# Performance work log

Measured on AMD Instinct MI355X. Metric: run time of the kernel, lower is better.

## Reference

```python
import jax, jax.numpy as jnp
import numpy as np
from functools import partial

V, BS, L, H, C = 50257, 1024, 6, 12, 768
HD = C // H

def _ln(x, w, b):
    mu = jnp.mean(x, axis=-1, keepdims=True)
    var = jnp.var(x, axis=-1, keepdims=True)
    return (x - mu) * jax.lax.rsqrt(var + 1e-5) * w + b

def setup_inputs() -> dict:
    key = jax.random.key(0)
    ks = jax.random.split(key, 12)
    s = 0.02
    inp = {
        "idx": jax.random.randint(ks[0], (4, 1024), 0, V, dtype=jnp.int32),
        "wte": jax.random.normal(ks[1], (V, C), jnp.float32) * s,
        "wpe": jax.random.normal(ks[2], (BS, C), jnp.float32) * s,
        # per-block stacked params; linear weights stored [in, out]
        "ln1_w": jnp.ones((L, C)), "ln1_b": jnp.zeros((L, C)),
        "attn_w": jax.random.normal(ks[3], (L, C, 3 * C), jnp.float32) * s,
        "attn_b": jnp.zeros((L, 3 * C)),
        "proj_w": jax.random.normal(ks[4], (L, C, C), jnp.float32) * s,
        "proj_b": jnp.zeros((L, C)),
        "ln2_w": jnp.ones((L, C)), "ln2_b": jnp.zeros((L, C)),
        "fc_w": jax.random.normal(ks[5], (L, C, 4 * C), jnp.float32) * s,
        "fc_b": jnp.zeros((L, 4 * C)),
        "fc2_w": jax.random.normal(ks[6], (L, 4 * C, C), jnp.float32) * s,
        "fc2_b": jnp.zeros((L, C)),
        "lnf_w": jnp.ones((C,)), "lnf_b": jnp.zeros((C,)),
    }
    return inp

def _forward(idx, wte, wpe, ln1_w, ln1_b, attn_w, attn_b, proj_w, proj_b,
             ln2_w, ln2_b, fc_w, fc_b, fc2_w, fc2_b, lnf_w, lnf_b):
    B, T = idx.shape
    x = wte[idx] + wpe[:T]  # [B,T,C]
    causal = jnp.tril(jnp.ones((T, T), bool))  # [T,T]
    scale = 1.0 / np.sqrt(HD)
    neg_inf = jnp.finfo(x.dtype).min

    def block(x, p):
        l1w, l1b, aw, ab, pw, pb, l2w, l2b, fw, fb, f2w, f2b = p
        h = _ln(x, l1w, l1b)
        qkv = h @ aw + ab  # [B,T,3C]
        q, k, v = jnp.split(qkv, 3, axis=-1)
        q = q.reshape(B, T, H, HD)
        k = k.reshape(B, T, H, HD)
        v = v.reshape(B, T, H, HD)
        att = jnp.einsum('bqhd,bkhd->bhqk', q, k) * scale
        att = jnp.where(causal, att, neg_inf)
        att = jax.nn.softmax(att, axis=-1)
        y = jnp.einsum('bhqk,bkhd->bqhd', att, v).reshape(B, T, C)
        x = x + y @ pw + pb
        h = _ln(x, l2w, l2b)
        h = jax.nn.gelu(h @ fw + fb, approximate=False)  # torch nn.GELU default = exact
        x = x + h @ f2w + f2b
        return x, None

    params = (ln1_w, ln1_b, attn_w, attn_b, proj_w, proj_b,
              ln2_w, ln2_b, fc_w, fc_b, fc2_w, fc2_b)
    x, _ = jax.lax.scan(block, x, params)
    x = _ln(x, lnf_w, lnf_b)
    logits = x @ wte.T  # tied lm_head, no bias
    return logits

def reference(idx, wte, wpe, ln1_w, ln1_b, attn_w, attn_b, proj_w, proj_b,
              ln2_w, ln2_b, fc_w, fc_b, fc2_w, fc2_b, lnf_w, lnf_b):
    return _forward(idx, wte, wpe, ln1_w, ln1_b, attn_w, attn_b, proj_w, proj_b,
                    ln2_w, ln2_b, fc_w, fc_b, fc2_w, fc2_b, lnf_w, lnf_b)
```

## Files before the change

### kernel.cpp

```cpp
#include <hip/hip_runtime.h>

#define BT     4096
#define CDIM   768
#define NLAYER 6
#define NHEAD  12
#define VREAL  50257
#define VPAD   50304

typedef __bf16 bf16x8 __attribute__((ext_vector_type(8)));
typedef float  f32x4  __attribute__((ext_vector_type(4)));

__device__ __forceinline__ unsigned short f2bf(float f) {
    unsigned int u = __builtin_bit_cast(unsigned int, f);
    u += 0x7fffu + ((u >> 16) & 1u);
    return (unsigned short)(u >> 16);
}

__global__ __launch_bounds__(256) void transpose_conv(
    const float* __restrict__ in, unsigned short* __restrict__ out, int K, int N)
{
    in  += (size_t)blockIdx.z * K * N;
    out += (size_t)blockIdx.z * K * N;
    __shared__ float t[32][33];
    int j0 = blockIdx.x * 32;
    int i0 = blockIdx.y * 32;
    int c = threadIdx.x;
    int r = threadIdx.y;
    #pragma unroll
    for (int rr = r; rr < 32; rr += 8)
        t[rr][c] = in[(size_t)(i0 + rr) * N + j0 + c];
    __syncthreads();
    #pragma unroll
    for (int rr = r; rr < 32; rr += 8)
        out[(size_t)(j0 + rr) * K + i0 + c] = f2bf(t[c][rr]);
}

__global__ __launch_bounds__(256) void wteconv(
    const float* __restrict__ wte, unsigned short* __restrict__ out)
{
    size_t e = ((size_t)blockIdx.x * 256 + threadIdx.x) * 4;
    int row = (int)(e / CDIM);
    int col = (int)(e % CDIM);
    ushort4 o;
    if (row < VREAL) {
        float4 v = *(const float4*)(wte + (size_t)row * CDIM + col);
        o.x = f2bf(v.x); o.y = f2bf(v.y); o.z = f2bf(v.z); o.w = f2bf(v.w);
    } else {
        o.x = 0; o.y = 0; o.z = 0; o.w = 0;
    }
    *(ushort4*)(out + e) = o;
}

__global__ __launch_bounds__(256) void embed_kernel(
    const int* __restrict__ idx, const float* __restrict__ wte,
    const float* __restrict__ wpe, float* __restrict__ x)
{
    int row = blockIdx.x;
    int t = row & 1023;
    int id = idx[row];
    const float* s = wte + (size_t)id * CDIM;
    const float* p = wpe + (size_t)t * CDIM;
    float* o = x + (size_t)row * CDIM;
    for (int c = threadIdx.x; c < CDIM; c += 256) o[c] = s[c] + p[c];
}

__global__ __launch_bounds__(256) void ln_kernel(
    const float* __restrict__ x, const float* __restrict__ w,
    const float* __restrict__ b, unsigned short* __restrict__ out)
{
    int row = blockIdx.x * 4 + (threadIdx.x >> 6);
    int lane = threadIdx.x & 63;
    const float* xp = x + (size_t)row * CDIM;
    float v[12];
    float s = 0.f, sq = 0.f;
    #pragma unroll
    for (int j = 0; j < 12; ++j) {
        float t = xp[j * 64 + lane];
        v[j] = t; s += t; sq += t * t;
    }
    #pragma unroll
    for (int o = 32; o > 0; o >>= 1) {
        s  += __shfl_xor(s, o, 64);
        sq += __shfl_xor(sq, o, 64);
    }
    float mu  = s * (1.f / CDIM);
    float var = sq * (1.f / CDIM) - mu * mu;
    float rs  = rsqrtf(var + 1e-5f);
    unsigned short* op = out + (size_t)row * CDIM;
    #pragma unroll
    for (int j = 0; j < 12; ++j) {
        int c = j * 64 + lane;
        op[c] = f2bf((v[j] - mu) * rs * w[c] + b[c]);
    }
}

template<int MODE>
__global__ __launch_bounds__(256) void gemm_kernel(
    const unsigned short* __restrict__ A, const unsigned short* __restrict__ Bt,
    const float* __restrict__ bias, const float* __restrict__ resid,
    float* __restrict__ outF, unsigned short* __restrict__ outB,
    unsigned short* __restrict__ qout, unsigned short* __restrict__ kout,
    unsigned short* __restrict__ vtout,
    int K, int Nout)
{
    __shared__ alignas(16) unsigned short As[4096];
    __shared__ alignas(16) unsigned short Bs[4096];
    const int tid  = threadIdx.x;
    const int wv   = tid >> 6;
    const int lane = tid & 63;
    const int m0 = blockIdx.x * 128;
    const int n0 = blockIdx.y * 128;
    const int wr = wv >> 1, wc = wv & 1;
    const int srow = lane >> 2;
    const int skk  = (lane & 3) * 8;
    const int fr = lane & 15;
    const int fk = (lane >> 4) * 8;

    f32x4 acc[4][4];
    #pragma unroll
    for (int i = 0; i < 4; ++i)
        #pragma unroll
        for (int j = 0; j < 4; ++j) acc[i][j] = f32x4{0.f, 0.f, 0.f, 0.f};

    for (int k0 = 0; k0 < K; k0 += 32) {
        #pragma unroll
        for (int j = 0; j < 2; ++j) {
            int row = j * 64 + wv * 16 + srow;
            const unsigned short* ga = A  + (size_t)(m0 + row) * K + k0 + skk;
            const unsigned short* gb = Bt + (size_t)(n0 + row) * K + k0 + skk;
            unsigned short* la = &As[j * 2048 + wv * 512];
            unsigned short* lb = &Bs[j * 2048 + wv * 512];
            __builtin_amdgcn_global_load_lds(
                (const __attribute__((address_space(1))) unsigned int*)ga,
                (__attribute__((address_space(3))) unsigned int*)la, 16, 0, 0);
            __builtin_amdgcn_global_load_lds(
                (const __attribute__((address_space(1))) unsigned int*)gb,
                (__attribute__((address_space(3))) unsigned int*)lb, 16, 0, 0);
        }
        __syncthreads();
        bf16x8 a[4], bb[4];
        #pragma unroll
        for (int m = 0; m < 4; ++m)
            a[m] = *(const bf16x8*)&As[(wr * 64 + m * 16 + fr) * 32 + fk];
        #pragma unroll
        for (int n = 0; n < 4; ++n)
            bb[n] = *(const bf16x8*)&Bs[(wc * 64 + n * 16 + fr) * 32 + fk];
        #pragma unroll
        for (int m = 0; m < 4; ++m)
            #pragma unroll
            for (int n = 0; n < 4; ++n)
                acc[m][n] = __builtin_amdgcn_mfma_f32_16x16x32_bf16(
                    a[m], bb[n], acc[m][n], 0, 0, 0);
        __syncthreads();
    }

    const int colb = n0 + wc * 64 + fr;
    const int rowb = m0 + wr * 64 + (lane >> 4) * 4;
    #pragma unroll
    for (int m = 0; m < 4; ++m) {
        #pragma unroll
        for (int n = 0; n < 4; ++n) {
            int col = colb + n * 16;
            int which = col / 768;
            int hh = (col - which * 768) >> 6;
            int dd = col & 63;
            #pragma unroll
            for (int r = 0; r < 4; ++r) {
                int row = rowb + m * 16 + r;
                float v = acc[m][n][r];
                if (MODE == 1) {
                    outF[(size_t)row * Nout + col] =
                        resid[(size_t)row * Nout + col] + v + bias[col];
                } else if (MODE == 2) {
                    float u = v + bias[col];
                    float g = 0.5f * u * (1.f + erff(u * 0.70710678118654752f));
                    outB[(size_t)row * Nout + col] = f2bf(g);
                } else if (MODE == 3) {
                    if (col < Nout) outF[(size_t)row * Nout + col] = v;
                } else if (MODE == 4) {
                    int bb2 = row >> 10, tt = row & 1023;
                    unsigned short val = f2bf(v + bias[col]);
                    if (which == 0)
                        qout[(((size_t)bb2 * NHEAD + hh) * 1024 + tt) * 64 + dd] = val;
                    else if (which == 1)
                        kout[(((size_t)bb2 * NHEAD + hh) * 1024 + tt) * 64 + dd] = val;
                    else
                        vtout[(((size_t)bb2 * NHEAD + hh) * 64 + dd) * 1024 + tt] = val;
                }
            }
        }
    }
}

__global__ __launch_bounds__(256) void attn_mfma_kernel(
    const unsigned short* __restrict__ qb, const unsigned short* __restrict__ kb,
    const unsigned short* __restrict__ vtb, unsigned short* __restrict__ y)
{
    __shared__ alignas(16) unsigned short Ps[4][16][72];
    const int qt = 15 - blockIdx.x;
    const int h = blockIdx.y, b = blockIdx.z;
    const int w = threadIdx.x >> 6, lane = threadIdx.x & 63;
    const int fr = lane & 15;
    const int fg = lane >> 4;
    const size_t bh = (size_t)(b * NHEAD + h);
    const unsigned short* Qb = qb  + bh * 1024 * 64;
    const unsigned short* Kb = kb  + bh * 1024 * 64;
    const unsigned short* Vt = vtb + bh * 64 * 1024;
    const int q0 = qt * 64 + w * 16;

    bf16x8 aq[2];
    aq[0] = *(const bf16x8*)(Qb + (size_t)(q0 + fr) * 64 + fg * 8);
    aq[1] = *(const bf16x8*)(Qb + (size_t)(q0 + fr) * 64 + 32 + fg * 8);

    f32x4 o[4];
    #pragma unroll
    for (int c = 0; c < 4; ++c) o[c] = f32x4{0.f, 0.f, 0.f, 0.f};
    float m[4], l[4];
    #pragma unroll
    for (int r = 0; r < 4; ++r) { m[r] = -1e30f; l[r] = 0.f; }

    for (int kt = 0; kt <= qt; ++kt) {
        const unsigned short* Kt = Kb + (size_t)kt * 64 * 64;
        f32x4 s[4];
        #pragma unroll
        for (int c = 0; c < 4; ++c) {
            bf16x8 bk0 = *(const bf16x8*)(Kt + (size_t)(c * 16 + fr) * 64 + fg * 8);
            bf16x8 bk1 = *(const bf16x8*)(Kt + (size_t)(c * 16 + fr) * 64 + 32 + fg * 8);
            s[c] = f32x4{0.f, 0.f, 0.f, 0.f};
            s[c] = __builtin_amdgcn_mfma_f32_16x16x32_bf16(aq[0], bk0, s[c], 0, 0, 0);
            s[c] = __builtin_amdgcn_mfma_f32_16x16x32_bf16(aq[1], bk1, s[c], 0, 0, 0);
        }
        float sc[4][4];
        #pragma unroll
        for (int c = 0; c < 4; ++c)
            #pragma unroll
            for (int r = 0; r < 4; ++r) {
                float v = s[c][r] * 0.125f;
                if (kt == qt && (kt * 64 + c * 16 + fr) > (q0 + fg * 4 + r))
                    v = -1e30f;
                sc[c][r] = v;
            }
        #pragma unroll
        for (int r = 0; r < 4; ++r) {
            float tm = fmaxf(fmaxf(sc[0][r], sc[1][r]), fmaxf(sc[2][r], sc[3][r]));
            tm = fmaxf(tm, __shfl_xor(tm, 1, 64));
            tm = fmaxf(tm, __shfl_xor(tm, 2, 64));
            tm = fmaxf(tm, __shfl_xor(tm, 4, 64));
            tm = fmaxf(tm, __shfl_xor(tm, 8, 64));
            float mn = fmaxf(m[r], tm);
            float corr = __expf(m[r] - mn);
            m[r] = mn;
            float ps = 0.f;
            #pragma unroll
            for (int c = 0; c < 4; ++c) {
                float p = __expf(sc[c][r] - mn);
                sc[c][r] = p;
                ps += p;
            }
            ps += __shfl_xor(ps, 1, 64);
            ps += __shfl_xor(ps, 2, 64);
            ps += __shfl_xor(ps, 4, 64);
            ps += __shfl_xor(ps, 8, 64);
            l[r] = l[r] * corr + ps;
            #pragma unroll
            for (int c = 0; c < 4; ++c) o[c][r] *= corr;
            #pragma unroll
            for (int c = 0; c < 4; ++c)
                Ps[w][fg * 4 + r][c * 16 + fr] = f2bf(sc[c][r]);
        }
        asm volatile("s_waitcnt lgkmcnt(0)" ::: "memory");
        bf16x8 ap0 = *(const bf16x8*)&Ps[w][fr][fg * 8];
        bf16x8 ap1 = *(const bf16x8*)&Ps[w][fr][32 + fg * 8];
        #pragma unroll
        for (int c = 0; c < 4; ++c) {
            const unsigned short* vb = Vt + (size_t)(c * 16 + fr) * 1024 + kt * 64;
            bf16x8 bv0 = *(const bf16x8*)(vb + fg * 8);
            bf16x8 bv1 = *(const bf16x8*)(vb + 32 + fg * 8);
            o[c] = __builtin_amdgcn_mfma_f32_16x16x32_bf16(ap0, bv0, o[c], 0, 0, 0);
            o[c] = __builtin_amdgcn_mfma_f32_16x16x32_bf16(ap1, bv1, o[c], 0, 0, 0);
        }
        asm volatile("s_waitcnt lgkmcnt(0)" ::: "memory");
    }

    float inv[4];
    #pragma unroll
    for (int r = 0; r < 4; ++r) inv[r] = 1.f / l[r];
    #pragma unroll
    for (int c = 0; c < 4; ++c)
        #pragma unroll
        for (int r = 0; r < 4; ++r) {
            int q = q0 + fg * 4 + r;
            y[((size_t)(b * 1024 + q)) * CDIM + h * 64 + c * 16 + fr] =
                f2bf(o[c][r] * inv[r]);
        }
}

extern "C" void kernel_launch(void* const* d_in, const int* in_sizes, int n_in,
                              void* d_out, int out_size, void* d_ws, size_t ws_size,
                              hipStream_t stream) {
    (void)in_sizes; (void)n_in; (void)out_size; (void)ws_size;
    const int*   idx   = (const int*)  d_in[0];
    const float* wte   = (const float*)d_in[1];
    const float* wpe   = (const float*)d_in[2];
    const float* ln1w  = (const float*)d_in[3];
    const float* ln1b  = (const float*)d_in[4];
    const float* attnw = (const float*)d_in[5];
    const float* attnb = (const float*)d_in[6];
    const float* projw = (const float*)d_in[7];
    const float* projb = (const float*)d_in[8];
    const float* ln2w  = (const float*)d_in[9];
    const float* ln2b  = (const float*)d_in[10];
    const float* fcw   = (const float*)d_in[11];
    const float* fcb   = (const float*)d_in[12];
    const float* fc2w  = (const float*)d_in[13];
    const float* fc2b  = (const float*)d_in[14];
    const float* lnfw  = (const float*)d_in[15];
    const float* lnfb  = (const float*)d_in[16];
    float* out = (float*)d_out;

    char* ws = (char*)d_ws;
    size_t off = 0;
    auto alloc = [&](size_t bytes) {
        void* p = ws + off;
        off += (bytes + 255) & ~(size_t)255;
        return p;
    };
    float*          x      = (float*)         alloc((size_t)BT * CDIM * 4);
    unsigned short* hbuf   = (unsigned short*)alloc((size_t)BT * CDIM * 2);
    unsigned short* qbuf   = (unsigned short*)alloc((size_t)BT * CDIM * 2);
    unsigned short* kbuf   = (unsigned short*)alloc((size_t)BT * CDIM * 2);
    unsigned short* vtbuf  = (unsigned short*)alloc((size_t)BT * CDIM * 2);
    unsigned short* ybuf   = (unsigned short*)alloc((size_t)BT * CDIM * 2);
    unsigned short* fcact  = (unsigned short*)alloc((size_t)BT * 4 * CDIM * 2);
    unsigned short* wqkvT  = (unsigned short*)alloc((size_t)NLAYER * 3 * CDIM * CDIM * 2);
    unsigned short* wprojT = (unsigned short*)alloc((size_t)NLAYER * CDIM * CDIM * 2);
    unsigned short* wfcT   = (unsigned short*)alloc((size_t)NLAYER * 4 * CDIM * CDIM * 2);
    unsigned short* wfc2T  = (unsigned short*)alloc((size_t)NLAYER * 4 * CDIM * CDIM * 2);
    unsigned short* wteB   = (unsigned short*)alloc((size_t)VPAD * CDIM * 2);

    transpose_conv<<<dim3(3*CDIM/32,   CDIM/32, NLAYER), dim3(32,8), 0, stream>>>(attnw, wqkvT, CDIM, 3*CDIM);
    transpose_conv<<<dim3(  CDIM/32,   CDIM/32, NLAYER), dim3(32,8), 0, stream>>>(projw, wprojT, CDIM, CDIM);
    transpose_conv<<<dim3(4*CDIM/32,   CDIM/32, NLAYER), dim3(32,8), 0, stream>>>(fcw,  wfcT,  CDIM, 4*CDIM);
    transpose_conv<<<dim3(  CDIM/32, 4*CDIM/32, NLAYER), dim3(32,8), 0, stream>>>(fc2w, wfc2T, 4*CDIM, CDIM);
    wteconv<<<(VPAD * CDIM / 4) / 256, 256, 0, stream>>>(wte, wteB);
    embed_kernel<<<BT, 256, 0, stream>>>(idx, wte, wpe, x);

    for (int l = 0; l < NLAYER; ++l) {
        ln_kernel<<<BT/4, 256, 0, stream>>>(x, ln1w + l*CDIM, ln1b + l*CDIM, hbuf);
        gemm_kernel<4><<<dim3(BT/128, 3*CDIM/128), 256, 0, stream>>>(
            hbuf, wqkvT + (size_t)l*3*CDIM*CDIM, attnb + (size_t)l*3*CDIM,
            nullptr, nullptr, nullptr, qbuf, kbuf, vtbuf, CDIM, 3*CDIM);
        attn_mfma_kernel<<<dim3(16, NHEAD, 4), 256, 0, stream>>>(qbuf, kbuf, vtbuf, ybuf);
        gemm_kernel<1><<<dim3(BT/128, CDIM/128), 256, 0, stream>>>(
            ybuf, wprojT + (size_t)l*CDIM*CDIM, projb + (size_t)l*CDIM,
            x, x, nullptr, nullptr, nullptr, nullptr, CDIM, CDIM);
        ln_kernel<<<BT/4, 256, 0, stream>>>(x, ln2w + l*CDIM, ln2b + l*CDIM, hbuf);
        gemm_kernel<2><<<dim3(BT/128, 4*CDIM/128), 256, 0, stream>>>(
            hbuf, wfcT + (size_t)l*4*CDIM*CDIM, fcb + (size_t)l*4*CDIM,
            nullptr, nullptr, fcact, nullptr, nullptr, nullptr, CDIM, 4*CDIM);
        gemm_kernel<1><<<dim3(BT/128, CDIM/128), 256, 0, stream>>>(
            fcact, wfc2T + (size_t)l*4*CDIM*CDIM, fc2b + (size_t)l*CDIM,
            x, x, nullptr, nullptr, nullptr, nullptr, 4*CDIM, CDIM);
    }
    ln_kernel<<<BT/4, 256, 0, stream>>>(x, lnfw, lnfb, hbuf);
    gemm_kernel<3><<<dim3(BT/128, VPAD/128), 256, 0, stream>>>(
        hbuf, wteB, nullptr, nullptr, out, nullptr, nullptr, nullptr, nullptr, CDIM, VREAL);
}
```

Baseline: 2.404 ms.

## Add double-buffered 256x256 LM-head GEMM, pipeline all GEMMs, swizzle block order

Adds a new 256x256-tile GEMM kernel with 512 threads for the vocabulary projection and pads the vocabulary to a multiple of 256. All GEMMs now double-buffer their LDS tiles so the next K-tile's global-to-LDS load is issued before the current tile's MFMAs. A block-index swizzle remaps workgroup order to group tiles across XCDs for better L2 locality. Larger tiles raise arithmetic intensity for the dominant LM-head GEMM, at the cost of more LDS per block and possibly lower occupancy.

```diff
diff --git a/kernel.cpp b/kernel.cpp
--- a/kernel.cpp
+++ b/kernel.cpp
@@ -5,7 +5,7 @@
 #define NLAYER 6
 #define NHEAD  12
 #define VREAL  50257
-#define VPAD   50304
+#define VPAD   50432
 
 typedef __bf16 bf16x8 __attribute__((ext_vector_type(8)));
 typedef float  f32x4  __attribute__((ext_vector_type(4)));
@@ -14,6 +14,18 @@
     unsigned int u = __builtin_bit_cast(unsigned int, f);
     u += 0x7fffu + ((u >> 16) & 1u);
     return (unsigned short)(u >> 16);
+}
+
+__device__ __forceinline__ void swz_block(int &bx, int &by) {
+    int gx = gridDim.x;
+    int nwg = gx * gridDim.y;
+    if ((nwg & 7) == 0) {
+        int lin = by * gx + bx;
+        int q = nwg >> 3;
+        lin = (lin & 7) * q + (lin >> 3);
+        bx = lin % gx;
+        by = lin / gx;
+    }
 }
 
 __global__ __launch_bounds__(256) void transpose_conv(
@@ -103,48 +115,58 @@
     unsigned short* __restrict__ vtout,
     int K, int Nout)
 {
-    __shared__ alignas(16) unsigned short As[4096];
-    __shared__ alignas(16) unsigned short Bs[4096];
+    __shared__ alignas(16) unsigned short As[2][4096];
+    __shared__ alignas(16) unsigned short Bs[2][4096];
     const int tid  = threadIdx.x;
     const int wv   = tid >> 6;
     const int lane = tid & 63;
-    const int m0 = blockIdx.x * 128;
-    const int n0 = blockIdx.y * 128;
+    int bx = blockIdx.x, by = blockIdx.y;
+    swz_block(bx, by);
+    const int m0 = bx * 128;
+    const int n0 = by * 128;
     const int wr = wv >> 1, wc = wv & 1;
     const int srow = lane >> 2;
     const int skk  = (lane & 3) * 8;
     const int fr = lane & 15;
     const int fk = (lane >> 4) * 8;
 
-    f32x4 acc[4][4];
-    #pragma unroll
-    for (int i = 0; i < 4; ++i)
-        #pragma unroll
-        for (int j = 0; j < 4; ++j) acc[i][j] = f32x4{0.f, 0.f, 0.f, 0.f};
-
-    for (int k0 = 0; k0 < K; k0 += 32) {
+    auto stage = [&](int k0, int bb) {
         #pragma unroll
         for (int j = 0; j < 2; ++j) {
             int row = j * 64 + wv * 16 + srow;
             const unsigned short* ga = A  + (size_t)(m0 + row) * K + k0 + skk;
             const unsigned short* gb = Bt + (size_t)(n0 + row) * K + k0 + skk;
-            unsigned short* la = &As[j * 2048 + wv * 512];
-            unsigned short* lb = &Bs[j * 2048 + wv * 512];
             __builtin_amdgcn_global_load_lds(
                 (const __attribute__((address_space(1))) unsigned int*)ga,
-                (__attribute__((address_space(3))) unsigned int*)la, 16, 0, 0);
+                (__attribute__((address_space(3))) unsigned int*)&As[bb][j * 2048 + wv * 512],
+                16, 0, 0);
             __builtin_amdgcn_global_load_lds(
                 (const __attribute__((address_space(1))) unsigned int*)gb,
-                (__attribute__((address_space(3))) unsigned int*)lb, 16, 0, 0);
-        }
-        __syncthreads();
+                (__attribute__((address_space(3))) unsigned int*)&Bs[bb][j * 2048 + wv * 512],
+                16, 0, 0);
+        }
+    };
+
+    f32x4 acc[4][4];
+    #pragma unroll
+    for (int i = 0; i < 4; ++i)
+        #pragma unroll
+        for (int j = 0; j < 4; ++j) acc[i][j] = f32x4{0.f, 0.f, 0.f, 0.f};
+
+    stage(0, 0);
+    __syncthreads();
+
+    const int nt = K >> 5;
+    for (int t = 0; t < nt; ++t) {
+        const int cb = t & 1;
+        if (t + 1 < nt) stage((t + 1) << 5, cb ^ 1);
         bf16x8 a[4], bb[4];
         #pragma unroll
         for (int m = 0; m < 4; ++m)
-            a[m] = *(const bf16x8*)&As[(wr * 64 + m * 16 + fr) * 32 + fk];
+            a[m] = *(const bf16x8*)&As[cb][(wr * 64 + m * 16 + fr) * 32 + fk];
         #pragma unroll
         for (int n = 0; n < 4; ++n)
-            bb[n] = *(const bf16x8*)&Bs[(wc * 64 + n * 16 + fr) * 32 + fk];
+            bb[n] = *(const bf16x8*)&Bs[cb][(wc * 64 + n * 16 + fr) * 32 + fk];
         #pragma unroll
         for (int m = 0; m < 4; ++m)
             #pragma unroll
@@ -175,8 +197,6 @@
                     float u = v + bias[col];
                     float g = 0.5f * u * (1.f + erff(u * 0.70710678118654752f));
                     outB[(size_t)row * Nout + col] = f2bf(g);
-                } else if (MODE == 3) {
-                    if (col < Nout) outF[(size_t)row * Nout + col] = v;
                 } else if (MODE == 4) {
                     int bb2 = row >> 10, tt = row & 1023;
                     unsigned short val = f2bf(v + bias[col]);
@@ -186,6 +206,93 @@
                         kout[(((size_t)bb2 * NHEAD + hh) * 1024 + tt) * 64 + dd] = val;
                     else
                         vtout[(((size_t)bb2 * NHEAD + hh) * 64 + dd) * 1024 + tt] = val;
+                }
+            }
+        }
+    }
+}
+
+__global__ __launch_bounds__(512, 2) void gemm256_kernel(
+    const unsigned short* __restrict__ A, const unsigned short* __restrict__ Bt,
+    float* __restrict__ outF, int K, int Nout)
+{
+    __shared__ alignas(16) unsigned short ldsA[2][16384];
+    __shared__ alignas(16) unsigned short ldsB[2][16384];
+    const int tid  = threadIdx.x;
+    const int wid  = tid >> 6;
+    const int lane = tid & 63;
+    int bx = blockIdx.x, by = blockIdx.y;
+    swz_block(bx, by);
+    const int m0 = bx * 256;
+    const int n0 = by * 256;
+    const int wm = wid >> 2;
+    const int wn = wid & 3;
+    const int srow = wid * 8 + (lane >> 3);
+    const int scol = (lane & 7) * 8;
+    const int fr = lane & 15;
+    const int fg = lane >> 4;
+
+    auto stage = [&](int kt, int bb) {
+        const int k0 = kt * 64;
+        #pragma unroll
+        for (int j = 0; j < 4; ++j) {
+            const unsigned short* ga = A  + (size_t)(m0 + j * 64 + srow) * K + k0 + scol;
+            const unsigned short* gb = Bt + (size_t)(n0 + j * 64 + srow) * K + k0 + scol;
+            __builtin_amdgcn_global_load_lds(
+                (const __attribute__((address_space(1))) unsigned int*)ga,
+                (__attribute__((address_space(3))) unsigned int*)&ldsA[bb][j * 4096 + wid * 512],
+                16, 0, 0);
+            __builtin_amdgcn_global_load_lds(
+                (const __attribute__((address_space(1))) unsigned int*)gb,
+                (__attribute__((address_space(3))) unsigned int*)&ldsB[bb][j * 4096 + wid * 512],
+                16, 0, 0);
+        }
+    };
+
+    f32x4 acc[8][4];
+    #pragma unroll
+    for (int i = 0; i < 8; ++i)
+        #pragma unroll
+        for (int j = 0; j < 4; ++j) acc[i][j] = f32x4{0.f, 0.f, 0.f, 0.f};
+
+    stage(0, 0);
+    __syncthreads();
+
+    const int nt = K >> 6;
+    for (int t = 0; t < nt; ++t) {
+        const int cb = t & 1;
+        if (t + 1 < nt) stage(t + 1, cb ^ 1);
+        #pragma unroll
+        for (int ks = 0; ks < 2; ++ks) {
+            bf16x8 a[8], b[4];
+            #pragma unroll
+            for (int m = 0; m < 8; ++m)
+                a[m] = *(const bf16x8*)&ldsA[cb][(wm * 128 + m * 16 + fr) * 64 + ks * 32 + fg * 8];
+            #pragma unroll
+            for (int n = 0; n < 4; ++n)
+                b[n] = *(const bf16x8*)&ldsB[cb][(wn * 64 + n * 16 + fr) * 64 + ks * 32 + fg * 8];
+            #pragma unroll
+            for (int m = 0; m < 8; ++m)
+                #pragma unroll
+                for (int n = 0; n < 4; ++n)
+                    acc[m][n] = __builtin_amdgcn_mfma_f32_16x16x32_bf16(
+                        a[m], b[n], acc[m][n], 0, 0, 0);
+        }
+        __syncthreads();
+    }
+
+    const int colb = n0 + wn * 64 + fr;
+    const int rowb = m0 + wm * 128 + fg * 4;
+    #pragma unroll
+    for (int m = 0; m < 8; ++m) {
+        #pragma unroll
+        for (int n = 0; n < 4; ++n) {
+            int col = colb + n * 16;
+            if (col < Nout) {
+                #pragma unroll
+                for (int r = 0; r < 4; ++r) {
+                    int row = rowb + m * 16 + r;
+                    outF[(size_t)row * Nout + col] = acc[m][n][r];
                 }
             }
         }
@@ -363,6 +470,6 @@
             x, x, nullptr, nullptr, nullptr, nullptr, 4*CDIM, CDIM);
     }
     ln_kernel<<<BT/4, 256, 0, stream>>>(x, lnfw, lnfb, hbuf);
-    gemm_kernel<3><<<dim3(BT/128, VPAD/128), 256, 0, stream>>>(
-        hbuf, wteB, nullptr, nullptr, out, nullptr, nullptr, nullptr, nullptr, CDIM, VREAL);
-}
+    gemm256_kernel<<<dim3(BT/256, VPAD/256), 512, 0, stream>>>(
+        hbuf, wteB, out, CDIM, VREAL);
+}
```

Result: no change. 2.451 ms (+2.0%).

## Add dedicated double-buffered LM-head GEMM kernel with swizzled LDS and block remap

Applied to the files above, without the earlier changes.

Replaces the generic gemm for the tied LM head with a specialized 512-thread kernel using 128x256 tiles. The A tile is double-buffered in LDS with XOR swizzling, and B fragments are loaded directly into registers and prefetched one step ahead. It also uses explicit waitcnt/barrier pipelining, setprio around MFMA bursts, and a workgroup remap across XCDs to improve L2 reuse. Vocabulary padding grows to a multiple of 256, which adds a little wasted compute and relies on the wteB buffer being allocated to the new VPAD size.

```diff
diff --git a/kernel.cpp b/kernel.cpp
--- a/kernel.cpp
+++ b/kernel.cpp
@@ -5,7 +5,7 @@
 #define NLAYER 6
 #define NHEAD  12
 #define VREAL  50257
-#define VPAD   50304
+#define VPAD   50432
 
 typedef __bf16 bf16x8 __attribute__((ext_vector_type(8)));
 typedef float  f32x4  __attribute__((ext_vector_type(4)));
@@ -14,6 +14,24 @@
     unsigned int u = __builtin_bit_cast(unsigned int, f);
     u += 0x7fffu + ((u >> 16) & 1u);
     return (unsigned short)(u >> 16);
+}
+
+__device__ __forceinline__ void gload16(const unsigned short* g, unsigned short* l) {
+    __builtin_amdgcn_global_load_lds(
+        (const __attribute__((address_space(1))) unsigned int*)g,
+        (__attribute__((address_space(3))) unsigned int*)l, 16, 0, 0);
+}
+
+__device__ __forceinline__ void swz_block(int &bx, int &by) {
+    int gx = gridDim.x;
+    int nwg = gx * gridDim.y;
+    if ((nwg & 7) == 0) {
+        int lin = by * gx + bx;
+        int q = nwg >> 3;
+        lin = (lin & 7) * q + (lin >> 3);
+        bx = lin % gx;
+        by = lin / gx;
+    }
 }
 
 __global__ __launch_bounds__(256) void transpose_conv(
@@ -126,16 +144,8 @@
         #pragma unroll
         for (int j = 0; j < 2; ++j) {
             int row = j * 64 + wv * 16 + srow;
-            const unsigned short* ga = A  + (size_t)(m0 + row) * K + k0 + skk;
-            const unsigned short* gb = Bt + (size_t)(n0 + row) * K + k0 + skk;
-            unsigned short* la = &As[j * 2048 + wv * 512];
-            unsigned short* lb = &Bs[j * 2048 + wv * 512];
-            __builtin_amdgcn_global_load_lds(
-                (const __attribute__((address_space(1))) unsigned int*)ga,
-                (__attribute__((address_space(3))) unsigned int*)la, 16, 0, 0);
-            __builtin_amdgcn_global_load_lds(
-                (const __attribute__((address_space(1))) unsigned int*)gb,
-                (__attribute__((address_space(3))) unsigned int*)lb, 16, 0, 0);
+            gload16(A  + (size_t)(m0 + row) * K + k0 + skk, &As[j * 2048 + wv * 512]);
+            gload16(Bt + (size_t)(n0 + row) * K + k0 + skk, &Bs[j * 2048 + wv * 512]);
         }
         __syncthreads();
         bf16x8 a[4], bb[4];
@@ -175,8 +185,6 @@
                     float u = v + bias[col];
                     float g = 0.5f * u * (1.f + erff(u * 0.70710678118654752f));
                     outB[(size_t)row * Nout + col] = f2bf(g);
-                } else if (MODE == 3) {
-                    if (col < Nout) outF[(size_t)row * Nout + col] = v;
                 } else if (MODE == 4) {
                     int bb2 = row >> 10, tt = row & 1023;
                     unsigned short val = f2bf(v + bias[col]);
@@ -186,6 +194,119 @@
                         kout[(((size_t)bb2 * NHEAD + hh) * 1024 + tt) * 64 + dd] = val;
                     else
                         vtout[(((size_t)bb2 * NHEAD + hh) * 64 + dd) * 1024 + tt] = val;
+                }
+            }
+        }
+    }
+}
+
+__global__ __launch_bounds__(512, 4) void lmhead_kernel(
+    const unsigned short* __restrict__ A, const unsigned short* __restrict__ Bt,
+    float* __restrict__ outF)
+{
+    __shared__ alignas(16) unsigned short ldsA[2][8192];
+    const int tid  = threadIdx.x;
+    const int wid  = tid >> 6;
+    const int lane = tid & 63;
+    const int fr = lane & 15, fg = lane >> 4;
+    int bx = blockIdx.x, by = blockIdx.y;
+    swz_block(bx, by);
+    const int m0 = bx * 128;
+    const int n0 = by * 256;
+
+    const int sr  = tid >> 3;
+    const int sks = ((tid & 7) * 8) ^ ((sr & 7) << 3);
+    const int wbase = wid * 512;
+
+    const unsigned short* Bw = Bt + (size_t)(n0 + wid * 32 + fr) * 768 + fg * 8;
+
+    const int arow = fr * 64;
+    const int swz0 = (fg * 8) ^ ((fr & 7) << 3);
+    const int swz1 = (32 + fg * 8) ^ ((fr & 7) << 3);
+
+    f32x4 acc[8][2];
+    #pragma unroll
+    for (int m = 0; m < 8; ++m)
+        #pragma unroll
+        for (int n = 0; n < 2; ++n) acc[m][n] = f32x4{0.f, 0.f, 0.f, 0.f};
+
+    bf16x8 brE[2][2], brO[2][2];
+
+#define LM_STAGE_A(t, buf)                                                    \
+    {                                                                         \
+        const int k0_ = (t) * 64;                                             \
+        gload16(A + (size_t)(m0 +      sr) * 768 + k0_ + sks,                 \
+                &ldsA[buf][wbase]);                                           \
+        gload16(A + (size_t)(m0 + 64 + sr) * 768 + k0_ + sks,                 \
+                &ldsA[buf][4096 + wbase]);                                    \
+    }
+#define LM_LOAD_B(t, br)                                                      \
+    {                                                                         \
+        const int k0_ = (t) * 64;                                             \
+        br[0][0] = *(const bf16x8*)(Bw + k0_);                                \
+        br[0][1] = *(const bf16x8*)(Bw + k0_ + 32);                           \
+        br[1][0] = *(const bf16x8*)(Bw + (size_t)16 * 768 + k0_);             \
+        br[1][1] = *(const bf16x8*)(Bw + (size_t)16 * 768 + k0_ + 32);        \
+    }
+#define LM_COMPUTE(buf, br)                                                   \
+    {                                                                         \
+        _Pragma("unroll")                                                     \
+        for (int m = 0; m < 8; ++m) {                                         \
+            bf16x8 a0 = *(const bf16x8*)&ldsA[buf][m * 1024 + arow + swz0];   \
+            bf16x8 a1 = *(const bf16x8*)&ldsA[buf][m * 1024 + arow + swz1];   \
+            acc[m][0] = __builtin_amdgcn_mfma_f32_16x16x32_bf16(a0, br[0][0], acc[m][0], 0, 0, 0); \
+            acc[m][1] = __builtin_amdgcn_mfma_f32_16x16x32_bf16(a0, br[1][0], acc[m][1], 0, 0, 0); \
+            acc[m][0] = __builtin_amdgcn_mfma_f32_16x16x32_bf16(a1, br[0][1], acc[m][0], 0, 0, 0); \
+            acc[m][1] = __builtin_amdgcn_mfma_f32_16x16x32_bf16(a1, br[1][1], acc[m][1], 0, 0, 0); \
+        }                                                                     \
+    }
+
+    LM_STAGE_A(0, 0);
+    LM_LOAD_B(0, brE);
+
+    #pragma unroll 1
+    for (int tt = 0; tt < 12; tt += 2) {
+        LM_STAGE_A(tt + 1, 1);
+        LM_LOAD_B(tt + 1, brO);
+        asm volatile("s_waitcnt vmcnt(6)" ::: "memory");
+        __builtin_amdgcn_s_barrier();
+        __builtin_amdgcn_s_setprio(1);
+        LM_COMPUTE(0, brE);
+        __builtin_amdgcn_s_setprio(0);
+        asm volatile("s_waitcnt lgkmcnt(0)" ::: "memory");
+        __builtin_amdgcn_sched_barrier(0);
+        __builtin_amdgcn_s_barrier();
+        if (tt + 2 < 12) {
+            LM_STAGE_A(tt + 2, 0);
+            LM_LOAD_B(tt + 2, brE);
+            asm volatile("s_waitcnt vmcnt(6)" ::: "memory");
+        } else {
+            asm volatile("s_waitcnt vmcnt(0)" ::: "memory");
+        }
+        __builtin_amdgcn_s_barrier();
+        __builtin_amdgcn_s_setprio(1);
+        LM_COMPUTE(1, brO);
+        __builtin_amdgcn_s_setprio(0);
+        asm volatile("s_waitcnt lgkmcnt(0)" ::: "memory");
+        __builtin_amdgcn_sched_barrier(0);
+        __builtin_amdgcn_s_barrier();
+    }
+#undef LM_STAGE_A
+#undef LM_LOAD_B
+#undef LM_COMPUTE
+
+    const int colb = n0 + wid * 32 + fr;
+    const int rowb = m0 + fg * 4;
+    #pragma unroll
+    for (int m = 0; m < 8; ++m) {
+        #pragma unroll
+        for (int n = 0; n < 2; ++n) {
+            int col = colb + n * 16;
+            if (col < VREAL) {
+                #pragma unroll
+                for (int r = 0; r < 4; ++r) {
+                    int row = rowb + m * 16 + r;
+                    outF[(size_t)row * VREAL + col] = acc[m][n][r];
                 }
             }
         }
@@ -363,6 +484,5 @@
             x, x, nullptr, nullptr, nullptr, nullptr, 4*CDIM, CDIM);
     }
     ln_kernel<<<BT/4, 256, 0, stream>>>(x, lnfw, lnfb, hbuf);
-    gemm_kernel<3><<<dim3(BT/128, VPAD/128), 256, 0, stream>>>(
-        hbuf, wteB, nullptr, nullptr, out, nullptr, nullptr, nullptr, nullptr, CDIM, VREAL);
-}
+    lmhead_kernel<<<dim3(BT/128, VPAD/256), 512, 0, stream>>>(hbuf, wteB, out);
+}
```

After: 2.363 ms. About the same (-1.7%).
